# Optimization experiments

Hardware: AMD Instinct MI355X
Metric: run time of the kernel (lower is better)

The kernel has to match this reference:

```python
import jax, jax.numpy as jnp
import numpy as np

N = 100000
IN_F = 165
HID = 128
E = 1600000


def gcn_conv(x, W, b, src, dst, n):
    # PyG GCNConv: h = x @ W; add self-loops; symmetric norm D^-1/2 A D^-1/2; aggregate; + bias
    h = x @ W  # [n, out]
    src_sl = jnp.concatenate([src, jnp.arange(n)])
    dst_sl = jnp.concatenate([dst, jnp.arange(n)])
    deg = jax.ops.segment_sum(jnp.ones_like(src_sl, dtype=h.dtype), dst_sl, num_segments=n)
    dinv = jnp.where(deg > 0, jax.lax.rsqrt(deg), 0.0)
    norm = dinv[src_sl] * dinv[dst_sl]  # [e+n]
    msg = h[src_sl] * norm[:, None]
    out = jax.ops.segment_sum(msg, dst_sl, num_segments=n)
    return out + b


def setup_inputs() -> dict:
    key = jax.random.key(0)
    k = jax.random.split(key, 8)
    x = jax.random.normal(k[0], (N, IN_F), dtype=jnp.float32)
    edge_index = jax.random.randint(k[1], (2, E), 0, N)
    s1 = 1.0 / np.sqrt(IN_F)
    s2 = 1.0 / np.sqrt(HID)
    W1 = jax.random.uniform(k[2], (IN_F, HID), jnp.float32, -s1, s1)
    b1 = jnp.zeros((HID,), jnp.float32)
    W2 = jax.random.uniform(k[3], (HID, HID), jnp.float32, -s2, s2)
    b2 = jnp.zeros((HID,), jnp.float32)
    Wc = jax.random.uniform(k[4], (HID, 2), jnp.float32, -s2, s2)
    bc = jax.random.uniform(k[5], (2,), jnp.float32, -s2, s2)
    return {"x": x, "edge_index": edge_index, "W1": W1, "b1": b1,
            "W2": W2, "b2": b2, "Wc": Wc, "bc": bc}


def reference(x, edge_index, W1, b1, W2, b2, Wc, bc):
    src, dst = edge_index[0], edge_index[1]
    h = jax.nn.relu(gcn_conv(x, W1, b1, src, dst, N))
    # dropout inactive (eval mode)
    h = jax.nn.relu(gcn_conv(h, W2, b2, src, dst, N))
    return h @ Wc + bc
```

## Files before the change

### kernel.cpp

```cpp
#include <hip/hip_runtime.h>


typedef _Float16 half8 __attribute__((ext_vector_type(8)));
typedef float floatx4 __attribute__((ext_vector_type(4)));
typedef float f4u __attribute__((ext_vector_type(4), aligned(4)));

#define SLOT_C 64
#define BCAP 4608
#define NBKT 391
#define CHUNK 4096

__global__ __launch_bounds__(256) void multisplit_k(const int* __restrict__ src,
                                                    const int* __restrict__ dst, int e,
                                                    int* __restrict__ bcnt,
                                                    int2* __restrict__ edges2) {
  __shared__ int lhist[NBKT];
  __shared__ int lbase[NBKT];
  __shared__ int lcur[NBKT];
  int t = threadIdx.x;
  int e0 = blockIdx.x * CHUNK;
  int e1 = min(e0 + CHUNK, e);
  for (int b = t; b < NBKT; b += 256) { lhist[b] = 0; lcur[b] = 0; }
  __syncthreads();
  for (int i = e0 + t; i < e1; i += 256)
    atomicAdd(&lhist[dst[i] >> 8], 1);
  __syncthreads();
  for (int b = t; b < NBKT; b += 256) {
    int h = lhist[b];
    lbase[b] = h ? atomicAdd(&bcnt[b], h) : 0;
  }
  __syncthreads();
  for (int i = e0 + t; i < e1; i += 256) {
    int d = dst[i];
    int b = d >> 8;
    int p = lbase[b] + atomicAdd(&lcur[b], 1);
    if (p < BCAP) edges2[(size_t)b * BCAP + p] = make_int2(src[i], d);
  }
}

__global__ __launch_bounds__(256) void csr_from_bins_k(const int2* __restrict__ edges2,
                                                       const int* __restrict__ bcnt,
                                                       int* __restrict__ cnt_g,
                                                       int* __restrict__ csr,
                                                       float* __restrict__ dinv, int n) {
  __shared__ int lcnt[256];
  int b = blockIdx.x;
  int node0 = b << 8;
  int t = threadIdx.x;
  lcnt[t] = 0;
  __syncthreads();
  int ec = min(bcnt[b], BCAP);
  const int2* ebase = edges2 + (size_t)b * BCAP;
  for (int i = t; i < ec; i += 256) {
    int2 ed = ebase[i];
    int p = atomicAdd(&lcnt[ed.y - node0], 1);
    if (p < SLOT_C) csr[((size_t)ed.y << 6) + p] = ed.x;
  }
  __syncthreads();
  int node = node0 + t;
  if (node < n) {
    int c = lcnt[t];
    cnt_g[node] = c;
    dinv[node] = rsqrtf((float)(c + 1));
  }
}

__global__ void w_split_k(const float* __restrict__ W, int K, int Kpad,
                          _Float16* __restrict__ WhT, _Float16* __restrict__ WlT) {
  int idx = blockIdx.x * blockDim.x + threadIdx.x;
  if (idx >= 128 * Kpad) return;
  int c = idx / Kpad, k = idx - c * Kpad;
  float v = (k < K) ? W[(size_t)k * 128 + c] : 0.f;
  _Float16 h = (_Float16)v;
  WhT[idx] = h;
  WlT[idx] = (_Float16)(v - (float)h);
}

template <bool AHALF>
__global__ __launch_bounds__(256) void gemm_f16_k(const void* __restrict__ Av,
                                                  const _Float16* __restrict__ WhT,
                                                  const _Float16* __restrict__ WlT,
                                                  const float* __restrict__ rowscale,
                                                  _Float16* __restrict__ out,
                                                  int n, int K, int Kpad) {
  int wave = threadIdx.x >> 6, lane = threadIdx.x & 63;
  int m = lane & 15, quad = lane >> 4;
  int rowbase = blockIdx.x * 128 + wave * 32;
  int ra[2];
  ra[0] = min(rowbase + m, n - 1);
  ra[1] = min(rowbase + 16 + m, n - 1);

  floatx4 acc[2][8];
#pragma unroll
  for (int t = 0; t < 2; ++t)
#pragma unroll
    for (int j = 0; j < 8; ++j) acc[t][j] = (floatx4){0.f, 0.f, 0.f, 0.f};

  int nslab = (K + 31) >> 5;
  for (int s = 0; s < nslab; ++s) {
    int kt = s << 5;
    int k0 = kt + quad * 8;
    bool tail = (kt + 32 > K);

    half8 ah[2], al[2];
#pragma unroll
    for (int t = 0; t < 2; ++t) {
      if (AHALF) {
        const _Float16* arow = (const _Float16*)Av + (size_t)ra[t] * K;
        if (!tail) {
          ah[t] = *(const half8*)(arow + k0);
        } else {
#pragma unroll
          for (int j = 0; j < 8; ++j) {
            int kk = k0 + j;
            kk = kk < K ? kk : K - 1;
            ah[t][j] = arow[kk];
          }
        }
      } else {
        const float* arow = (const float*)Av + (size_t)ra[t] * K;
        float v[8];
        if (!tail) {
          f4u x0 = *(const f4u*)(arow + k0);
          f4u x1 = *(const f4u*)(arow + k0 + 4);
          v[0] = x0.x; v[1] = x0.y; v[2] = x0.z; v[3] = x0.w;
          v[4] = x1.x; v[5] = x1.y; v[6] = x1.z; v[7] = x1.w;
        } else {
#pragma unroll
          for (int j = 0; j < 8; ++j) {
            int kk = k0 + j;
            kk = kk < K ? kk : K - 1;
            v[j] = arow[kk];
          }
        }
#pragma unroll
        for (int j = 0; j < 8; ++j) {
          _Float16 h = (_Float16)v[j];
          ah[t][j] = h;
          al[t][j] = (_Float16)(v[j] - (float)h);
        }
      }
    }

#pragma unroll
    for (int g = 0; g < 2; ++g) {
      half8 wh[4], wl[4];
#pragma unroll
      for (int c = 0; c < 4; ++c) {
        size_t o = (size_t)((g * 4 + c) * 16 + m) * Kpad + k0;
        wh[c] = *(const half8*)(WhT + o);
        wl[c] = *(const half8*)(WlT + o);
      }
#pragma unroll
      for (int c = 0; c < 4; ++c) {
        int ct = g * 4 + c;
#pragma unroll
        for (int t = 0; t < 2; ++t) {
          acc[t][ct] = __builtin_amdgcn_mfma_f32_16x16x32_f16(ah[t], wh[c], acc[t][ct], 0, 0, 0);
          acc[t][ct] = __builtin_amdgcn_mfma_f32_16x16x32_f16(ah[t], wl[c], acc[t][ct], 0, 0, 0);
          if (!AHALF)
            acc[t][ct] = __builtin_amdgcn_mfma_f32_16x16x32_f16(al[t], wh[c], acc[t][ct], 0, 0, 0);
        }
      }
    }
  }

#pragma unroll
  for (int t = 0; t < 2; ++t) {
#pragma unroll
    for (int i = 0; i < 4; ++i) {
      int row = rowbase + t * 16 + quad * 4 + i;
      if (row < n) {
        float di = rowscale ? rowscale[row] : 1.0f;
#pragma unroll
        for (int ct = 0; ct < 8; ++ct)
          out[(size_t)row * 128 + ct * 16 + m] = (_Float16)(acc[t][ct][i] * di);
      }
    }
  }
}

template <bool CLS>
__global__ __launch_bounds__(256) void aggregate_k(const _Float16* __restrict__ g,
                                                   const int* __restrict__ cnt,
                                                   const int* __restrict__ csr,
                                                   const float* __restrict__ dinv,
                                                   const float* __restrict__ bias,
                                                   const float* __restrict__ Wc,
                                                   const float* __restrict__ bc,
                                                   _Float16* __restrict__ out16,
                                                   float* __restrict__ out32, int n) {
  int wave = threadIdx.x >> 6;
  int lane = threadIdx.x & 63;
  int i = blockIdx.x * 4 + wave;
  if (i >= n) return;
  int qtr = lane >> 4;
  int l16 = lane & 15;
  int f = l16 * 8;

  float acc[8];
#pragma unroll
  for (int j = 0; j < 8; ++j) acc[j] = 0.f;

  int deg = min(cnt[i], SLOT_C);
  size_t s0 = (size_t)i << 6;

  if (deg > 0) {
    int last = deg - 1;
    for (int eb = 0; eb < deg; eb += 16) {
#pragma unroll
      for (int k = 0; k < 4; ++k) {
        int ee = eb + 4 * k + qtr;
        float w = (ee <= last) ? 1.f : 0.f;
        int ec = (ee <= last) ? ee : last;
        int srow = csr[s0 + ec];
        half8 v = *(const half8*)&g[(size_t)srow * 128 + f];
#pragma unroll
        for (int j = 0; j < 8; ++j) acc[j] = fmaf(w, (float)v[j], acc[j]);
      }
    }
#pragma unroll
    for (int j = 0; j < 8; ++j) {
      acc[j] += __shfl_xor(acc[j], 16, 64);
      acc[j] += __shfl_xor(acc[j], 32, 64);
    }
  }

  half8 self = *(const half8*)&g[(size_t)i * 128 + f];
  float di = dinv[i];
  float4 b0 = *(const float4*)&bias[f];
  float4 b1 = *(const float4*)&bias[f + 4];
  float bv[8] = {b0.x, b0.y, b0.z, b0.w, b1.x, b1.y, b1.z, b1.w};
  float r[8];
#pragma unroll
  for (int j = 0; j < 8; ++j)
    r[j] = fmaxf((acc[j] + (float)self[j]) * di + bv[j], 0.f);

  if (!CLS) {
    if (qtr == 0) {
      half8 o;
#pragma unroll
      for (int j = 0; j < 8; ++j) o[j] = (_Float16)(r[j] * di);
      *(half8*)&out16[(size_t)i * 128 + f] = o;
    }
  } else {
    float c0v = 0.f, c1v = 0.f;
#pragma unroll
    for (int q = 0; q < 4; ++q) {
      float4 wv = *(const float4*)&Wc[f * 2 + q * 4];
      c0v += r[q * 2] * wv.x + r[q * 2 + 1] * wv.z;
      c1v += r[q * 2] * wv.y + r[q * 2 + 1] * wv.w;
    }
#pragma unroll
    for (int off = 8; off > 0; off >>= 1) {
      c0v += __shfl_down(c0v, off, 16);
      c1v += __shfl_down(c1v, off, 16);
    }
    if (lane == 0) {
      out32[(size_t)i * 2 + 0] = c0v + bc[0];
      out32[(size_t)i * 2 + 1] = c1v + bc[1];
    }
  }
}

extern "C" void kernel_launch(void* const* d_in, const int* in_sizes, int n_in,
                              void* d_out, int out_size, void* d_ws, size_t ws_size,
                              hipStream_t stream) {
  const float* x  = (const float*)d_in[0];
  const int*   ei = (const int*)d_in[1];
  const float* W1 = (const float*)d_in[2];
  const float* b1 = (const float*)d_in[3];
  const float* W2 = (const float*)d_in[4];
  const float* b2 = (const float*)d_in[5];
  const float* Wc = (const float*)d_in[6];
  const float* bc = (const float*)d_in[7];
  float* out = (float*)d_out;

  const int IN_F = 165;
  const int KP1 = 192;
  const int n = in_sizes[0] / IN_F;
  const int e = in_sizes[1] / 2;
  const int* src = ei;
  const int* dst = ei + e;

  char* ws = (char*)d_ws;
  size_t off = 0;
  auto alloc = [&](size_t bytes) -> void* {
    void* p = ws + off;
    off += (bytes + 255) & ~(size_t)255;
    return p;
  };
  _Float16* bufA = (_Float16*)alloc((size_t)n * 128 * 2);
  _Float16* bufB = (_Float16*)alloc((size_t)n * 128 * 2);
  int*   csr  = (int*)alloc((size_t)n * SLOT_C * 4);
  int2*  edges2 = (int2*)alloc((size_t)NBKT * BCAP * 8);
  int*   cnt  = (int*)alloc((size_t)n * 4);
  int*   bcnt = (int*)alloc((size_t)NBKT * 4);
  float* dinv = (float*)alloc((size_t)n * 4);
  _Float16* w1h = (_Float16*)alloc((size_t)128 * KP1 * 2);
  _Float16* w1l = (_Float16*)alloc((size_t)128 * KP1 * 2);
  _Float16* w2h = (_Float16*)alloc((size_t)128 * 128 * 2);
  _Float16* w2l = (_Float16*)alloc((size_t)128 * 128 * 2);

  hipMemsetAsync(bcnt, 0, (size_t)NBKT * 4, stream);

  const int tb = 256;
  w_split_k<<<(128 * KP1 + tb - 1) / tb, tb, 0, stream>>>(W1, IN_F, KP1, w1h, w1l);
  w_split_k<<<(128 * 128 + tb - 1) / tb, tb, 0, stream>>>(W2, 128, 128, w2h, w2l);

  multisplit_k<<<(e + CHUNK - 1) / CHUNK, 256, 0, stream>>>(src, dst, e, bcnt, edges2);
  csr_from_bins_k<<<NBKT, 256, 0, stream>>>(edges2, bcnt, cnt, csr, dinv, n);

  gemm_f16_k<false><<<(n + 127) / 128, 256, 0, stream>>>(x, w1h, w1l, dinv, bufA, n, IN_F, KP1);
  aggregate_k<false><<<(n + 3) / 4, 256, 0, stream>>>(bufA, cnt, csr, dinv, b1, nullptr, nullptr,
                                                      bufB, nullptr, n);
  gemm_f16_k<true><<<(n + 127) / 128, 256, 0, stream>>>(bufB, w2h, w2l, nullptr, bufA, n, 128, 128);
  aggregate_k<true><<<(n + 3) / 4, 256, 0, stream>>>(bufA, cnt, csr, dinv, b2, Wc, bc,
                                                     nullptr, out, n);
}
```

Baseline: 377.6 us.

## Retile split-f16 GEMM to 64x64 blocks with software-prefetched A slabs

The MFMA GEMM kernel now gives each block 64 rows and half of the 128 output columns, selected by block-index parity. Each wave owns a 16x64 tile with 4 accumulators instead of 32x128 with 16. The K loop is unrolled by two, loading the next A slab while the current slab's MFMAs run. This lowers register pressure and doubles the grid, aiming for more occupancy and latency hiding. The cost is that every A row, including the fp32 input x, is read by two blocks, so correctness and speed depend on Kpad giving an even slab count and on those repeated reads hitting cache.

```diff
diff --git a/kernel.cpp b/kernel.cpp
--- a/kernel.cpp
+++ b/kernel.cpp
@@ -85,97 +85,92 @@
                                                   int n, int K, int Kpad) {
   int wave = threadIdx.x >> 6, lane = threadIdx.x & 63;
   int m = lane & 15, quad = lane >> 4;
-  int rowbase = blockIdx.x * 128 + wave * 32;
-  int ra[2];
-  ra[0] = min(rowbase + m, n - 1);
-  ra[1] = min(rowbase + 16 + m, n - 1);
-
-  floatx4 acc[2][8];
-#pragma unroll
-  for (int t = 0; t < 2; ++t)
-#pragma unroll
-    for (int j = 0; j < 8; ++j) acc[t][j] = (floatx4){0.f, 0.f, 0.f, 0.f};
-
-  int nslab = (K + 31) >> 5;
-  for (int s = 0; s < nslab; ++s) {
-    int kt = s << 5;
-    int k0 = kt + quad * 8;
-    bool tail = (kt + 32 > K);
-
-    half8 ah[2], al[2];
-#pragma unroll
-    for (int t = 0; t < 2; ++t) {
-      if (AHALF) {
-        const _Float16* arow = (const _Float16*)Av + (size_t)ra[t] * K;
-        if (!tail) {
-          ah[t] = *(const half8*)(arow + k0);
-        } else {
-#pragma unroll
-          for (int j = 0; j < 8; ++j) {
-            int kk = k0 + j;
-            kk = kk < K ? kk : K - 1;
-            ah[t][j] = arow[kk];
-          }
-        }
+  int rowblk = blockIdx.x >> 1;
+  int cbase = (blockIdx.x & 1) * 4;
+  int rowbase = rowblk * 64 + wave * 16;
+  int ra = min(rowbase + m, n - 1);
+
+  floatx4 acc[4];
+#pragma unroll
+  for (int c = 0; c < 4; ++c) acc[c] = (floatx4){0.f, 0.f, 0.f, 0.f};
+
+  const int nslab = Kpad >> 5;
+
+  f4u xa0, xa1, xb0, xb1;
+  half8 ha, hb;
+
+  auto loadA = [&](int s, f4u& x0, f4u& x1, half8& h) {
+    int k0 = (s << 5) + quad * 8;
+    if constexpr (AHALF) {
+      const _Float16* arow = (const _Float16*)Av + (size_t)ra * K;
+      h = *(const half8*)(arow + k0);
+    } else {
+      const float* arow = (const float*)Av + (size_t)ra * K;
+      if ((s << 5) + 32 <= K) {
+        x0 = *(const f4u*)(arow + k0);
+        x1 = *(const f4u*)(arow + k0 + 4);
       } else {
-        const float* arow = (const float*)Av + (size_t)ra[t] * K;
-        float v[8];
-        if (!tail) {
-          f4u x0 = *(const f4u*)(arow + k0);
-          f4u x1 = *(const f4u*)(arow + k0 + 4);
-          v[0] = x0.x; v[1] = x0.y; v[2] = x0.z; v[3] = x0.w;
-          v[4] = x1.x; v[5] = x1.y; v[6] = x1.z; v[7] = x1.w;
-        } else {
-#pragma unroll
-          for (int j = 0; j < 8; ++j) {
-            int kk = k0 + j;
-            kk = kk < K ? kk : K - 1;
-            v[j] = arow[kk];
-          }
-        }
-#pragma unroll
-        for (int j = 0; j < 8; ++j) {
-          _Float16 h = (_Float16)v[j];
-          ah[t][j] = h;
-          al[t][j] = (_Float16)(v[j] - (float)h);
-        }
+#pragma unroll
+        for (int j = 0; j < 4; ++j) { int kk = k0 + j;     kk = kk < K ? kk : K - 1; x0[j] = arow[kk]; }
+#pragma unroll
+        for (int j = 0; j < 4; ++j) { int kk = k0 + 4 + j; kk = kk < K ? kk : K - 1; x1[j] = arow[kk]; }
       }
     }
-
-#pragma unroll
-    for (int g = 0; g < 2; ++g) {
-      half8 wh[4], wl[4];
-#pragma unroll
-      for (int c = 0; c < 4; ++c) {
-        size_t o = (size_t)((g * 4 + c) * 16 + m) * Kpad + k0;
-        wh[c] = *(const half8*)(WhT + o);
-        wl[c] = *(const half8*)(WlT + o);
+  };
+
+  auto loadW = [&](int s, half8 (&wh)[4], half8 (&wl)[4]) {
+    int k0 = (s << 5) + quad * 8;
+#pragma unroll
+    for (int c = 0; c < 4; ++c) {
+      size_t o = (size_t)((cbase + c) * 16 + m) * Kpad + k0;
+      wh[c] = *(const half8*)(WhT + o);
+      wl[c] = *(const half8*)(WlT + o);
+    }
+  };
+
+  auto doSlab = [&](const half8 (&wh)[4], const half8 (&wl)[4],
+                    const f4u& x0, const f4u& x1, const half8& h) {
+    half8 ah, al;
+    if constexpr (AHALF) {
+      ah = h;
+    } else {
+#pragma unroll
+      for (int j = 0; j < 8; ++j) {
+        float v = (j < 4) ? x0[j] : x1[j - 4];
+        _Float16 hh = (_Float16)v;
+        ah[j] = hh;
+        al[j] = (_Float16)(v - (float)hh);
       }
-#pragma unroll
-      for (int c = 0; c < 4; ++c) {
-        int ct = g * 4 + c;
-#pragma unroll
-        for (int t = 0; t < 2; ++t) {
-          acc[t][ct] = __builtin_amdgcn_mfma_f32_16x16x32_f16(ah[t], wh[c], acc[t][ct], 0, 0, 0);
-          acc[t][ct] = __builtin_amdgcn_mfma_f32_16x16x32_f16(ah[t], wl[c], acc[t][ct], 0, 0, 0);
-          if (!AHALF)
-            acc[t][ct] = __builtin_amdgcn_mfma_f32_16x16x32_f16(al[t], wh[c], acc[t][ct], 0, 0, 0);
-        }
-      }
-    }
-  }
-
-#pragma unroll
-  for (int t = 0; t < 2; ++t) {
-#pragma unroll
-    for (int i = 0; i < 4; ++i) {
-      int row = rowbase + t * 16 + quad * 4 + i;
-      if (row < n) {
-        float di = rowscale ? rowscale[row] : 1.0f;
-#pragma unroll
-        for (int ct = 0; ct < 8; ++ct)
-          out[(size_t)row * 128 + ct * 16 + m] = (_Float16)(acc[t][ct][i] * di);
-      }
+    }
+#pragma unroll
+    for (int c = 0; c < 4; ++c) {
+      acc[c] = __builtin_amdgcn_mfma_f32_16x16x32_f16(ah, wh[c], acc[c], 0, 0, 0);
+      acc[c] = __builtin_amdgcn_mfma_f32_16x16x32_f16(ah, wl[c], acc[c], 0, 0, 0);
+      if constexpr (!AHALF)
+        acc[c] = __builtin_amdgcn_mfma_f32_16x16x32_f16(al, wh[c], acc[c], 0, 0, 0);
+    }
+  };
+
+  loadA(0, xa0, xa1, ha);
+  for (int s = 0; s < nslab; s += 2) {
+    half8 wh0[4], wl0[4];
+    loadW(s, wh0, wl0);
+    loadA(s + 1, xb0, xb1, hb);
+    doSlab(wh0, wl0, xa0, xa1, ha);
+    half8 wh1[4], wl1[4];
+    loadW(s + 1, wh1, wl1);
+    if (s + 2 < nslab) loadA(s + 2, xa0, xa1, ha);
+    doSlab(wh1, wl1, xb0, xb1, hb);
+  }
+
+#pragma unroll
+  for (int i = 0; i < 4; ++i) {
+    int row = rowbase + quad * 4 + i;
+    if (row < n) {
+      float di = rowscale ? rowscale[row] : 1.0f;
+#pragma unroll
+      for (int c = 0; c < 4; ++c)
+        out[(size_t)row * 128 + (cbase + c) * 16 + m] = (_Float16)(acc[c][i] * di);
     }
   }
 }
@@ -311,10 +306,11 @@
   multisplit_k<<<(e + CHUNK - 1) / CHUNK, 256, 0, stream>>>(src, dst, e, bcnt, edges2);
   csr_from_bins_k<<<NBKT, 256, 0, stream>>>(edges2, bcnt, cnt, csr, dinv, n);
 
-  gemm_f16_k<false><<<(n + 127) / 128, 256, 0, stream>>>(x, w1h, w1l, dinv, bufA, n, IN_F, KP1);
+  const int gemmgrid = 2 * ((n + 63) / 64);
+  gemm_f16_k<false><<<gemmgrid, 256, 0, stream>>>(x, w1h, w1l, dinv, bufA, n, IN_F, KP1);
   aggregate_k<false><<<(n + 3) / 4, 256, 0, stream>>>(bufA, cnt, csr, dinv, b1, nullptr, nullptr,
                                                       bufB, nullptr, n);
-  gemm_f16_k<true><<<(n + 127) / 128, 256, 0, stream>>>(bufB, w2h, w2l, nullptr, bufA, n, 128, 128);
+  gemm_f16_k<true><<<gemmgrid, 256, 0, stream>>>(bufB, w2h, w2l, nullptr, bufA, n, 128, 128);
   aggregate_k<true><<<(n + 3) / 4, 256, 0, stream>>>(bufA, cnt, csr, dinv, b2, Wc, bc,
                                                      nullptr, out, n);
 }
```

Result: slower. 415.3 us (+10.0%).

## Pre-swizzle weights into MFMA fragment layout and prefetch A slabs in GEMM

Applied to the files above, without the earlier changes.

Weight hi/lo splits are now written in a per-lane MFMA fragment order, so each lane loads its B fragments with contiguous coalesced half8 reads instead of strided transposed reads. The GEMM is templated on slab count with the K loop fully unrolled, and A-operand loads run two slabs ahead through a triple buffer to hide global latency behind the MFMAs. This raises register pressure, since 16 weight fragments plus the A buffers are live at once, which may reduce occupancy.

```diff
diff --git a/kernel.cpp b/kernel.cpp
--- a/kernel.cpp
+++ b/kernel.cpp
@@ -65,24 +65,28 @@
   }
 }
 
-__global__ void w_split_k(const float* __restrict__ W, int K, int Kpad,
-                          _Float16* __restrict__ WhT, _Float16* __restrict__ WlT) {
+__global__ void w_split_frag_k(const float* __restrict__ W, int K, int nslab,
+                               _Float16* __restrict__ WF) {
   int idx = blockIdx.x * blockDim.x + threadIdx.x;
-  if (idx >= 128 * Kpad) return;
-  int c = idx / Kpad, k = idx - c * Kpad;
-  float v = (k < K) ? W[(size_t)k * 128 + c] : 0.f;
+  if (idx >= nslab * 8192) return;
+  int j = idx & 7;
+  int lane = (idx >> 3) & 63;
+  int p = (idx >> 9) & 1;
+  int c = (idx >> 10) & 7;
+  int s = idx >> 13;
+  int k = (s << 5) + ((lane >> 4) << 3) + j;
+  int col = (c << 4) + (lane & 15);
+  float v = (k < K) ? W[(size_t)k * 128 + col] : 0.f;
   _Float16 h = (_Float16)v;
-  WhT[idx] = h;
-  WlT[idx] = (_Float16)(v - (float)h);
-}
-
-template <bool AHALF>
+  WF[idx] = p ? (_Float16)(v - (float)h) : h;
+}
+
+template <bool AHALF, int NSLAB>
 __global__ __launch_bounds__(256) void gemm_f16_k(const void* __restrict__ Av,
-                                                  const _Float16* __restrict__ WhT,
-                                                  const _Float16* __restrict__ WlT,
+                                                  const _Float16* __restrict__ WF,
                                                   const float* __restrict__ rowscale,
                                                   _Float16* __restrict__ out,
-                                                  int n, int K, int Kpad) {
+                                                  int n, int K) {
   int wave = threadIdx.x >> 6, lane = threadIdx.x & 63;
   int m = lane & 15, quad = lane >> 4;
   int rowbase = blockIdx.x * 128 + wave * 32;
@@ -94,75 +98,72 @@
 #pragma unroll
   for (int t = 0; t < 2; ++t)
 #pragma unroll
-    for (int j = 0; j < 8; ++j) acc[t][j] = (floatx4){0.f, 0.f, 0.f, 0.f};
-
-  int nslab = (K + 31) >> 5;
-  for (int s = 0; s < nslab; ++s) {
-    int kt = s << 5;
-    int k0 = kt + quad * 8;
-    bool tail = (kt + 32 > K);
-
-    half8 ah[2], al[2];
+    for (int c = 0; c < 8; ++c) acc[t][c] = (floatx4){0.f, 0.f, 0.f, 0.f};
+
+  f4u xb[3][2][2];
+  half8 hb[3][2];
+
+  auto loadA = [&](int s, int b) {
+    int k0 = (s << 5) + quad * 8;
 #pragma unroll
     for (int t = 0; t < 2; ++t) {
-      if (AHALF) {
+      if constexpr (AHALF) {
         const _Float16* arow = (const _Float16*)Av + (size_t)ra[t] * K;
-        if (!tail) {
-          ah[t] = *(const half8*)(arow + k0);
-        } else {
-#pragma unroll
-          for (int j = 0; j < 8; ++j) {
-            int kk = k0 + j;
-            kk = kk < K ? kk : K - 1;
-            ah[t][j] = arow[kk];
-          }
-        }
+        hb[b][t] = *(const half8*)(arow + k0);
       } else {
         const float* arow = (const float*)Av + (size_t)ra[t] * K;
-        float v[8];
-        if (!tail) {
-          f4u x0 = *(const f4u*)(arow + k0);
-          f4u x1 = *(const f4u*)(arow + k0 + 4);
-          v[0] = x0.x; v[1] = x0.y; v[2] = x0.z; v[3] = x0.w;
-          v[4] = x1.x; v[5] = x1.y; v[6] = x1.z; v[7] = x1.w;
+        if ((s << 5) + 32 <= K) {
+          xb[b][t][0] = *(const f4u*)(arow + k0);
+          xb[b][t][1] = *(const f4u*)(arow + k0 + 4);
         } else {
 #pragma unroll
-          for (int j = 0; j < 8; ++j) {
-            int kk = k0 + j;
-            kk = kk < K ? kk : K - 1;
-            v[j] = arow[kk];
-          }
+          for (int j = 0; j < 4; ++j) { int kk = k0 + j;     kk = kk < K ? kk : K - 1; xb[b][t][0][j] = arow[kk]; }
+#pragma unroll
+          for (int j = 0; j < 4; ++j) { int kk = k0 + 4 + j; kk = kk < K ? kk : K - 1; xb[b][t][1][j] = arow[kk]; }
         }
+      }
+    }
+  };
+
+  loadA(0, 0);
+  if (NSLAB > 1) loadA(1, 1);
+
+#pragma unroll
+  for (int s = 0; s < NSLAB; ++s) {
+    const _Float16* wbase = WF + (size_t)s * 8192;
+    half8 wh[8], wl[8];
+#pragma unroll
+    for (int c = 0; c < 8; ++c) {
+      wh[c] = *(const half8*)(wbase + c * 1024 + lane * 8);
+      wl[c] = *(const half8*)(wbase + c * 1024 + 512 + lane * 8);
+    }
+    if (s + 2 < NSLAB) loadA(s + 2, (s + 2) % 3);
+
+    int b = s % 3;
+    half8 ah[2], al[2];
+#pragma unroll
+    for (int t = 0; t < 2; ++t) {
+      if constexpr (AHALF) {
+        ah[t] = hb[b][t];
+      } else {
 #pragma unroll
         for (int j = 0; j < 8; ++j) {
-          _Float16 h = (_Float16)v[j];
-          ah[t][j] = h;
-          al[t][j] = (_Float16)(v[j] - (float)h);
+          float v = (j < 4) ? xb[b][t][0][j] : xb[b][t][1][j - 4];
+          _Float16 hh = (_Float16)v;
+          ah[t][j] = hh;
+          al[t][j] = (_Float16)(v - (float)hh);
         }
       }
     }
-
-#pragma unroll
-    for (int g = 0; g < 2; ++g) {
-      half8 wh[4], wl[4];
-#pragma unroll
-      for (int c = 0; c < 4; ++c) {
-        size_t o = (size_t)((g * 4 + c) * 16 + m) * Kpad + k0;
-        wh[c] = *(const half8*)(WhT + o);
-        wl[c] = *(const half8*)(WlT + o);
-      }
-#pragma unroll
-      for (int c = 0; c < 4; ++c) {
-        int ct = g * 4 + c;
-#pragma unroll
-        for (int t = 0; t < 2; ++t) {
-          acc[t][ct] = __builtin_amdgcn_mfma_f32_16x16x32_f16(ah[t], wh[c], acc[t][ct], 0, 0, 0);
-          acc[t][ct] = __builtin_amdgcn_mfma_f32_16x16x32_f16(ah[t], wl[c], acc[t][ct], 0, 0, 0);
-          if (!AHALF)
-            acc[t][ct] = __builtin_amdgcn_mfma_f32_16x16x32_f16(al[t], wh[c], acc[t][ct], 0, 0, 0);
-        }
-      }
-    }
+#pragma unroll
+    for (int c = 0; c < 8; ++c)
+#pragma unroll
+      for (int t = 0; t < 2; ++t) {
+        acc[t][c] = __builtin_amdgcn_mfma_f32_16x16x32_f16(ah[t], wh[c], acc[t][c], 0, 0, 0);
+        acc[t][c] = __builtin_amdgcn_mfma_f32_16x16x32_f16(ah[t], wl[c], acc[t][c], 0, 0, 0);
+        if constexpr (!AHALF)
+          acc[t][c] = __builtin_amdgcn_mfma_f32_16x16x32_f16(al[t], wh[c], acc[t][c], 0, 0, 0);
+      }
   }
 
 #pragma unroll
@@ -173,8 +174,8 @@
       if (row < n) {
         float di = rowscale ? rowscale[row] : 1.0f;
 #pragma unroll
-        for (int ct = 0; ct < 8; ++ct)
-          out[(size_t)row * 128 + ct * 16 + m] = (_Float16)(acc[t][ct][i] * di);
+        for (int c = 0; c < 8; ++c)
+          out[(size_t)row * 128 + c * 16 + m] = (_Float16)(acc[t][c][i] * di);
       }
     }
   }
@@ -277,7 +278,8 @@
   float* out = (float*)d_out;
 
   const int IN_F = 165;
-  const int KP1 = 192;
+  const int NS1 = 6;
+  const int NS2 = 4;
   const int n = in_sizes[0] / IN_F;
   const int e = in_sizes[1] / 2;
   const int* src = ei;
@@ -297,24 +299,22 @@
   int*   cnt  = (int*)alloc((size_t)n * 4);
   int*   bcnt = (int*)alloc((size_t)NBKT * 4);
   float* dinv = (float*)alloc((size_t)n * 4);
-  _Float16* w1h = (_Float16*)alloc((size_t)128 * KP1 * 2);
-  _Float16* w1l = (_Float16*)alloc((size_t)128 * KP1 * 2);
-  _Float16* w2h = (_Float16*)alloc((size_t)128 * 128 * 2);
-  _Float16* w2l = (_Float16*)alloc((size_t)128 * 128 * 2);
+  _Float16* wf1 = (_Float16*)alloc((size_t)NS1 * 8192 * 2);
+  _Float16* wf2 = (_Float16*)alloc((size_t)NS2 * 8192 * 2);
 
   hipMemsetAsync(bcnt, 0, (size_t)NBKT * 4, stream);
 
-  const int tb = 256;
-  w_split_k<<<(128 * KP1 + tb - 1) / tb, tb, 0, stream>>>(W1, IN_F, KP1, w1h, w1l);
-  w_split_k<<<(128 * 128 + tb - 1) / tb, tb, 0, stream>>>(W2, 128, 128, w2h, w2l);
+  w_split_frag_k<<<NS1 * 32, 256, 0, stream>>>(W1, IN_F, NS1, wf1);
+  w_split_frag_k<<<NS2 * 32, 256, 0, stream>>>(W2, 128, NS2, wf2);
 
   multisplit_k<<<(e + CHUNK - 1) / CHUNK, 256, 0, stream>>>(src, dst, e, bcnt, edges2);
   csr_from_bins_k<<<NBKT, 256, 0, stream>>>(edges2, bcnt, cnt, csr, dinv, n);
 
-  gemm_f16_k<false><<<(n + 127) / 128, 256, 0, stream>>>(x, w1h, w1l, dinv, bufA, n, IN_F, KP1);
+  const int gemmgrid = (n + 127) / 128;
+  gemm_f16_k<false, NS1><<<gemmgrid, 256, 0, stream>>>(x, wf1, dinv, bufA, n, IN_F);
   aggregate_k<false><<<(n + 3) / 4, 256, 0, stream>>>(bufA, cnt, csr, dinv, b1, nullptr, nullptr,
                                                       bufB, nullptr, n);
-  gemm_f16_k<true><<<(n + 127) / 128, 256, 0, stream>>>(bufB, w2h, w2l, nullptr, bufA, n, 128, 128);
+  gemm_f16_k<true, NS2><<<gemmgrid, 256, 0, stream>>>(bufB, wf2, nullptr, bufA, n, 128);
   aggregate_k<true><<<(n + 3) / 4, 256, 0, stream>>>(bufA, cnt, csr, dinv, b2, Wc, bc,
                                                      nullptr, out, n);
 }
```

New measurement: 338.0 us. 1.12x faster.
